# Kernel tuning notes

Hardware: AMD Instinct MI355X
Metric: run time of the kernel (lower is better)

Reference implementation:

```python
import jax, jax.numpy as jnp
import numpy as np

H = 4  # pairwise_num_attention_heads

def _layer_norm(x, gamma, beta, eps=1e-5):
    mu = jnp.mean(x, axis=-1, keepdims=True)
    var = jnp.var(x, axis=-1, keepdims=True)
    return (x - mu) * jax.lax.rsqrt(var + eps) * gamma + beta

def setup_inputs() -> dict:
    key = jax.random.key(0)
    ks = jax.random.split(key, 8)
    B, L, P = 1, 256, 128
    s = 0.02
    return {
        "pairwise_states": jax.random.normal(ks[0], (B, L, L, P), jnp.float32),
        "ln_gamma": jnp.ones((P,), jnp.float32),
        "ln_beta": jnp.zeros((P,), jnp.float32),
        "Wq": jax.random.normal(ks[1], (P, P), jnp.float32) * s,
        "Wk": jax.random.normal(ks[2], (P, P), jnp.float32) * s,
        "Wv": jax.random.normal(ks[3], (P, P), jnp.float32) * s,
        "Wb": jax.random.normal(ks[4], (P, H), jnp.float32) * s,
        "Wg": jax.random.normal(ks[5], (P, P), jnp.float32) * s,
        "bg": jnp.zeros((P,), jnp.float32),
        "Wo": jax.random.normal(ks[6], (P, P), jnp.float32) * s,
        "bo": jnp.zeros((P,), jnp.float32),
    }

def reference(pairwise_states, ln_gamma, ln_beta, Wq, Wk, Wv, Wb, Wg, bg, Wo, bo):
    # Row-axis triangle attention (RibonanzaNetPairwiseAttention, axis='row', eval mode).
    B, L, _, P = pairwise_states.shape
    D = P // H  # attention_head_size
    x = _layer_norm(pairwise_states, ln_gamma, ln_beta)  # [b,i,j,p]
    q = (x @ Wq).reshape(B, L, L, H, D)
    k = (x @ Wk).reshape(B, L, L, H, D)
    v = (x @ Wv).reshape(B, L, L, H, D)
    scale = jnp.asarray(D, x.dtype) ** 0.5
    # pairwise bias: [b,i,j,h] -> broadcast over the row axis of the scores
    bias = jnp.einsum('bijp,ph->bhij', x, Wb)  # [b,h,L,L]
    # scores[b,h,i,j,k]: within row i, query position j attends to key position k
    scores = jnp.einsum('bijhd,bikhd->bhijk', q, k) / scale + bias[:, :, None]
    probs = jax.nn.softmax(scores, axis=-1)
    ctx = jnp.einsum('bhijk,bikhd->bijhd', probs, v).reshape(B, L, L, P)
    gate = jax.nn.sigmoid(x @ Wg + bg)
    ctx = gate * ctx
    # output dense + residual (AxisDropout is identity in eval mode)
    return ctx @ Wo + bo + pairwise_states
```

## Files before the change

### kernel.cpp

```cpp
#include <hip/hip_runtime.h>

#define NPOS 65536

typedef __attribute__((ext_vector_type(8))) short bf16x8;
typedef __attribute__((ext_vector_type(4))) float f32x4;

#if __has_builtin(__builtin_amdgcn_exp2f)
#define EXP2F(x) __builtin_amdgcn_exp2f(x)
#else
#define EXP2F(x) __expf((x) * 0.6931471805599453f)
#endif
#if __has_builtin(__builtin_amdgcn_rcpf)
#define RCPF(x) __builtin_amdgcn_rcpf(x)
#else
#define RCPF(x) (1.0f / (x))
#endif

static __device__ __forceinline__ unsigned short f2bf(float f) {
  union { float f; unsigned int u; } v; v.f = f;
  unsigned int r = v.u + 0x7fffu + ((v.u >> 16) & 1u);
  return (unsigned short)(r >> 16);
}
static __device__ __forceinline__ float lo_bf(unsigned int u) {
  union { unsigned int u; float f; } v; v.u = u << 16; return v.f;
}
static __device__ __forceinline__ float hi_bf(unsigned int u) {
  union { unsigned int u; float f; } v; v.u = u & 0xffff0000u; return v.f;
}
static __device__ __forceinline__ unsigned int permpack(float hi, float lo) {
  union { float f; unsigned int u; } a, b;
  a.f = hi; b.f = lo;
#if __has_builtin(__builtin_amdgcn_perm)
  return __builtin_amdgcn_perm(a.u, b.u, 0x07060302u);
#else
  return (a.u & 0xffff0000u) | (b.u >> 16);
#endif
}

__global__ void k_pack(const float* __restrict__ Wq, const float* __restrict__ Wk,
                       const float* __restrict__ Wv, const float* __restrict__ Wg,
                       const float* __restrict__ Wo,
                       ushort* __restrict__ WT, ushort* __restrict__ WoT) {
  int idx = blockIdx.x * blockDim.x + threadIdx.x;
  if (idx < 512 * 128) {
    int n = idx >> 7, k = idx & 127;
    int nn = n & 127;
    float val;
    if (n < 128)      val = Wq[k * 128 + nn] * (0.17677669529663687f * 1.4426950408889634f);
    else if (n < 256) val = Wk[k * 128 + nn];
    else if (n < 384) val = Wv[k * 128 + nn];
    else              val = Wg[k * 128 + nn];
    WT[idx] = f2bf(val);
  } else if (idx < 512 * 128 + 128 * 128) {
    int j = idx - 512 * 128;
    int n = j >> 7, k = j & 127;
    WoT[j] = f2bf(Wo[k * 128 + n]);
  }
}

__global__ __launch_bounds__(128, 4) void k_ln(
    const float* __restrict__ in, const float* __restrict__ gamma,
    const float* __restrict__ beta, const float* __restrict__ Wb,
    ushort* __restrict__ xln, ushort* __restrict__ biasB) {
  int t = threadIdx.x, wv = t >> 6, lane = t & 63;
  int n = lane & 15, g = lane >> 4;
  int myrow = blockIdx.x * 32 + wv * 16 + n;
  const float* rp = in + (size_t)myrow * 128;

  float xv[32];
  float sm = 0.f, ssm = 0.f;
  #pragma unroll
  for (int kc = 0; kc < 4; kc++)
    #pragma unroll
    for (int pr = 0; pr < 2; pr++) {
      float4 v = *(const float4*)(rp + kc * 32 + g * 8 + pr * 4);
      int o = kc * 8 + pr * 4;
      xv[o] = v.x; xv[o+1] = v.y; xv[o+2] = v.z; xv[o+3] = v.w;
      sm  += v.x + v.y + v.z + v.w;
      ssm += v.x*v.x + v.y*v.y + v.z*v.z + v.w*v.w;
    }
  sm  += __shfl_xor(sm, 16, 64);  sm  += __shfl_xor(sm, 32, 64);
  ssm += __shfl_xor(ssm, 16, 64); ssm += __shfl_xor(ssm, 32, 64);
  float mu  = sm * (1.0f / 128.0f);
  float var = ssm * (1.0f / 128.0f) - mu * mu;
  float rs  = rsqrtf(var + 1e-5f);
  float p0 = 0.f, p1 = 0.f, p2 = 0.f, p3 = 0.f;
  #pragma unroll
  for (int kc = 0; kc < 4; kc++)
    #pragma unroll
    for (int pr = 0; pr < 2; pr++) {
      int c0 = kc * 32 + g * 8 + pr * 4;
      float4 g4 = *(const float4*)(gamma + c0);
      float4 b4 = *(const float4*)(beta + c0);
      int o = kc * 8 + pr * 4;
      #pragma unroll
      for (int r = 0; r < 4; r++) {
        float xn = (xv[o + r] - mu) * rs * (&g4.x)[r] + (&b4.x)[r];
        xv[o + r] = xn;
        float4 w = ((const float4*)Wb)[c0 + r];
        p0 += xn * w.x; p1 += xn * w.y; p2 += xn * w.z; p3 += xn * w.w;
      }
    }
  #pragma unroll
  for (int kc = 0; kc < 4; kc++)
    #pragma unroll
    for (int pr = 0; pr < 2; pr++) {
      int o = kc * 8 + pr * 4;
      uint2 px;
      px.x = (unsigned int)f2bf(xv[o]) | ((unsigned int)f2bf(xv[o + 1]) << 16);
      px.y = (unsigned int)f2bf(xv[o + 2]) | ((unsigned int)f2bf(xv[o + 3]) << 16);
      *(uint2*)(xln + (size_t)myrow * 128 + kc * 32 + g * 8 + pr * 4) = px;
    }
  p0 += __shfl_xor(p0, 16, 64); p0 += __shfl_xor(p0, 32, 64);
  p1 += __shfl_xor(p1, 16, 64); p1 += __shfl_xor(p1, 32, 64);
  p2 += __shfl_xor(p2, 16, 64); p2 += __shfl_xor(p2, 32, 64);
  p3 += __shfl_xor(p3, 16, 64); p3 += __shfl_xor(p3, 32, 64);
  if (g == 0) {
    const float l2e = 1.4426950408889634f;
    biasB[0 * NPOS + myrow] = f2bf(p0 * l2e);
    biasB[1 * NPOS + myrow] = f2bf(p1 * l2e);
    biasB[2 * NPOS + myrow] = f2bf(p2 * l2e);
    biasB[3 * NPOS + myrow] = f2bf(p3 * l2e);
  }
}

#define KS 36
#define VS 264
#define QS 36
__global__ __launch_bounds__(512, 3) void k_attn2(
    const ushort* __restrict__ xln, const ushort* __restrict__ WT,
    const float* __restrict__ bg, const ushort* __restrict__ biasB,
    ushort* __restrict__ gctx) {
  __shared__ __align__(16) ushort Klds[256 * KS];
  __shared__ __align__(16) ushort VTlds[32 * VS];
  __shared__ __align__(16) ushort qstg[8][32 * QS];
  int i = blockIdx.x & 255, h = blockIdx.x >> 8;
  int t = threadIdx.x, wv = t >> 6, lane = t & 63;
  int n = lane & 15, g = lane >> 4;
  int r0 = wv * 32;

  bf16x8 a[2][4];
  const ushort* xb = xln + ((size_t)i * 256 + r0) * 128;
  #pragma unroll
  for (int c = 0; c < 2; c++)
    #pragma unroll
    for (int kc = 0; kc < 4; kc++)
      a[c][kc] = *(const bf16x8*)(xb + (size_t)(c * 16 + n) * 128 + kc * 32 + g * 8);

  f32x4 gs[2][2];
  #pragma unroll
  for (int sect = 0; sect < 4; sect++) {
    bf16x8 b[2][4];
    #pragma unroll
    for (int ntl = 0; ntl < 2; ntl++)
      #pragma unroll
      for (int kc = 0; kc < 4; kc++)
        b[ntl][kc] = *(const bf16x8*)(WT + (size_t)(sect * 128 + h * 32 + ntl * 16 + n) * 128 + kc * 32 + g * 8);
    #pragma unroll
    for (int c = 0; c < 2; c++) {
      f32x4 acc[2];
      #pragma unroll
      for (int ntl = 0; ntl < 2; ntl++) {
        f32x4 cc = {0.f, 0.f, 0.f, 0.f};
        #pragma unroll
        for (int kc = 0; kc < 4; kc++)
          cc = __builtin_amdgcn_mfma_f32_16x16x32_bf16(a[c][kc], b[ntl][kc], cc, 0, 0, 0);
        acc[ntl] = cc;
      }
      if (sect == 0) {
        #pragma unroll
        for (int ntl = 0; ntl < 2; ntl++)
          #pragma unroll
          for (int r = 0; r < 4; r++)
            qstg[wv][(c * 16 + g * 4 + r) * QS + ntl * 16 + n] = f2bf(acc[ntl][r]);
      } else if (sect == 1) {
        #pragma unroll
        for (int ntl = 0; ntl < 2; ntl++)
          #pragma unroll
          for (int r = 0; r < 4; r++)
            Klds[(r0 + c * 16 + g * 4 + r) * KS + ntl * 16 + n] = f2bf(acc[ntl][r]);
      } else if (sect == 2) {
        #pragma unroll
        for (int ntl = 0; ntl < 2; ntl++) {
          uint2 vp;
          vp.x = (unsigned int)f2bf(acc[ntl][0]) | ((unsigned int)f2bf(acc[ntl][1]) << 16);
          vp.y = (unsigned int)f2bf(acc[ntl][2]) | ((unsigned int)f2bf(acc[ntl][3]) << 16);
          *(uint2*)(&VTlds[(ntl * 16 + n) * VS + r0 + c * 16 + g * 4]) = vp;
        }
      } else {
        #pragma unroll
        for (int ntl = 0; ntl < 2; ntl++)
          #pragma unroll
          for (int r = 0; r < 4; r++)
            gs[c][ntl][r] = 1.0f / (1.0f + __expf(-(acc[ntl][r] + bg[h * 32 + ntl * 16 + n])));
      }
    }
  }
  __syncthreads();

  const ushort* bb = biasB + (size_t)h * NPOS;
  #pragma unroll
  for (int tt = 0; tt < 2; tt++) {
    int j0 = r0 + tt * 16;
    union { bf16x8 v; uint2 u[2]; } bq;
    bq.u[0] = *(const uint2*)(&qstg[wv][(tt * 16 + n) * QS + g * 8]);
    bq.u[1] = *(const uint2*)(&qstg[wv][(tt * 16 + n) * QS + g * 8 + 4]);
    ushort* Pw = &qstg[wv][tt * 16 * QS];
    uint2 bv[16];
    #pragma unroll
    for (int kt = 0; kt < 16; kt++)
      bv[kt] = *(const uint2*)(bb + (size_t)(j0 + n) * 256 + kt * 16 + g * 4);
    f32x4 s[16];
    #pragma unroll
    for (int kt = 0; kt < 16; kt++) {
      union { bf16x8 v; uint2 u[2]; } ak;
      ak.u[0] = *(const uint2*)(&Klds[(kt * 16 + n) * KS + g * 8]);
      ak.u[1] = *(const uint2*)(&Klds[(kt * 16 + n) * KS + g * 8 + 4]);
      f32x4 cc;
      cc[0] = lo_bf(bv[kt].x); cc[1] = hi_bf(bv[kt].x);
      cc[2] = lo_bf(bv[kt].y); cc[3] = hi_bf(bv[kt].y);
      s[kt] = __builtin_amdgcn_mfma_f32_16x16x32_bf16(ak.v, bq.v, cc, 0, 0, 0);
    }
    f32x4 a4 = {0.f, 0.f, 0.f, 0.f};
    #pragma unroll
    for (int kt = 0; kt < 16; kt++) {
      #pragma unroll
      for (int r = 0; r < 4; r++) s[kt][r] = EXP2F(s[kt][r]);
      a4 += s[kt];
    }
    float smm = (a4[0] + a4[1]) + (a4[2] + a4[3]);
    smm += __shfl_xor(smm, 16, 64);
    smm += __shfl_xor(smm, 32, 64);
    float inv = RCPF(smm);
    f32x4 ctx0 = {0.f, 0.f, 0.f, 0.f}, ctx1 = {0.f, 0.f, 0.f, 0.f};
    #pragma unroll
    for (int c8 = 0; c8 < 8; c8++) {
      #pragma unroll
      for (int t2 = 0; t2 < 2; t2++) {
        int kt = c8 * 2 + t2;
        uint2 pp;
        pp.x = permpack(s[kt][1] * inv, s[kt][0] * inv);
        pp.y = permpack(s[kt][3] * inv, s[kt][2] * inv);
        *(uint2*)(&Pw[n * QS + t2 * 16 + g * 4]) = pp;
      }
      union { bf16x8 v; uint2 u[2]; } ap;
      ap.u[0] = *(const uint2*)(&Pw[n * QS + g * 8]);
      ap.u[1] = *(const uint2*)(&Pw[n * QS + g * 8 + 4]);
      bf16x8 v0 = *(const bf16x8*)(&VTlds[(size_t)n * VS + c8 * 32 + g * 8]);
      bf16x8 v1 = *(const bf16x8*)(&VTlds[(size_t)(16 + n) * VS + c8 * 32 + g * 8]);
      ctx0 = __builtin_amdgcn_mfma_f32_16x16x32_bf16(ap.v, v0, ctx0, 0, 0, 0);
      ctx1 = __builtin_amdgcn_mfma_f32_16x16x32_bf16(ap.v, v1, ctx1, 0, 0, 0);
    }
    #pragma unroll
    for (int r = 0; r < 4; r++) {
      size_t pos = (size_t)i * 256 + j0 + g * 4 + r;
      gctx[pos * 128 + h * 32 + n]      = f2bf(ctx0[r] * gs[tt][0][r]);
      gctx[pos * 128 + h * 32 + 16 + n] = f2bf(ctx1[r] * gs[tt][1][r]);
    }
  }
}

__global__ __launch_bounds__(256, 4) void k_out(
    const ushort* __restrict__ gctx, const ushort* __restrict__ WoT,
    const float* __restrict__ bo, const float* __restrict__ in0,
    float* __restrict__ out) {
  int t = threadIdx.x, wv = t >> 6, lane = t & 63;
  int n = lane & 15, g = lane >> 4;
  int row0 = blockIdx.x * 64 + wv * 16;
  bf16x8 cfr[4];
  #pragma unroll
  for (int kc = 0; kc < 4; kc++)
    cfr[kc] = *(const bf16x8*)(gctx + (size_t)(row0 + n) * 128 + kc * 32 + g * 8);
  size_t rowg = (size_t)row0 + n;
  #pragma unroll
  for (int ntl = 0; ntl < 8; ntl++) {
    f32x4 acc = {0.f, 0.f, 0.f, 0.f};
    #pragma unroll
    for (int kc = 0; kc < 4; kc++) {
      bf16x8 wo = *(const bf16x8*)(WoT + (size_t)(ntl * 16 + n) * 128 + kc * 32 + g * 8);
      acc = __builtin_amdgcn_mfma_f32_16x16x32_bf16(wo, cfr[kc], acc, 0, 0, 0);
    }
    f32x4 b4 = *(const f32x4*)(bo + ntl * 16 + g * 4);
    size_t o = rowg * 128 + ntl * 16 + g * 4;
    f32x4 r4 = *(const f32x4*)(in0 + o);
    acc[0] += b4[0] + r4[0]; acc[1] += b4[1] + r4[1];
    acc[2] += b4[2] + r4[2]; acc[3] += b4[3] + r4[3];
    *(f32x4*)(out + o) = acc;
  }
}

extern "C" void kernel_launch(void* const* d_in, const int* in_sizes, int n_in,
                              void* d_out, int out_size, void* d_ws, size_t ws_size,
                              hipStream_t stream) {
  const float* in0   = (const float*)d_in[0];
  const float* gamma = (const float*)d_in[1];
  const float* beta  = (const float*)d_in[2];
  const float* Wq    = (const float*)d_in[3];
  const float* Wk    = (const float*)d_in[4];
  const float* Wv    = (const float*)d_in[5];
  const float* Wb    = (const float*)d_in[6];
  const float* Wg    = (const float*)d_in[7];
  const float* bg    = (const float*)d_in[8];
  const float* Wo    = (const float*)d_in[9];
  const float* bo    = (const float*)d_in[10];
  float* out = (float*)d_out;
  char* ws = (char*)d_ws;

  const size_t MB = 1024 * 1024;
  ushort* gctx  = (ushort*)(ws);
  ushort* xln   = (ushort*)(ws + 16 * MB);
  ushort* biasB = (ushort*)(ws + 32 * MB);
  ushort* WT    = (ushort*)(ws + 33 * MB);
  ushort* WoT   = (ushort*)(ws + 33 * MB + 128 * 1024);

  k_pack <<<320, 256, 0, stream>>>(Wq, Wk, Wv, Wg, Wo, WT, WoT);
  k_ln   <<<2048, 128, 0, stream>>>(in0, gamma, beta, Wb, xln, biasB);
  k_attn2<<<1024, 512, 0, stream>>>(xln, WT, bg, biasB, gctx);
  k_out  <<<1024, 256, 0, stream>>>(gctx, WoT, bo, in0, out);
}
```

Baseline: 242.9 us.

## Keep Q in registers via transposed MFMA and shrink P staging

Computes the Q projection with swapped MFMA operands so its output lands directly in the register layout needed as the B operand for the scores MFMA. This removes the Q round trip through shared memory and its scalar stores. K is read with a permuted k-index layout (KS padded to 40) that stays consistent because the Q register packing matches. The P staging buffer shrinks to 16 rows with 16-byte loads. Occupancy hint drops from 3 to 2 blocks per SM, which may reduce latency hiding but allows more registers.

```diff
diff --git a/kernel.cpp b/kernel.cpp
--- a/kernel.cpp
+++ b/kernel.cpp
@@ -124,16 +124,16 @@
   }
 }
 
-#define KS 36
+#define KS 40
 #define VS 264
-#define QS 36
-__global__ __launch_bounds__(512, 3) void k_attn2(
+#define PST 40
+__global__ __launch_bounds__(512, 2) void k_attn2(
     const ushort* __restrict__ xln, const ushort* __restrict__ WT,
     const float* __restrict__ bg, const ushort* __restrict__ biasB,
     ushort* __restrict__ gctx) {
   __shared__ __align__(16) ushort Klds[256 * KS];
   __shared__ __align__(16) ushort VTlds[32 * VS];
-  __shared__ __align__(16) ushort qstg[8][32 * QS];
+  __shared__ __align__(16) ushort pstg[8][16 * PST];
   int i = blockIdx.x & 255, h = blockIdx.x >> 8;
   int t = threadIdx.x, wv = t >> 6, lane = t & 63;
   int n = lane & 15, g = lane >> 4;
@@ -147,6 +147,7 @@
     for (int kc = 0; kc < 4; kc++)
       a[c][kc] = *(const bf16x8*)(xb + (size_t)(c * 16 + n) * 128 + kc * 32 + g * 8);
 
+  bf16x8 qreg[2];
   f32x4 gs[2][2];
   #pragma unroll
   for (int sect = 0; sect < 4; sect++) {
@@ -163,16 +164,21 @@
       for (int ntl = 0; ntl < 2; ntl++) {
         f32x4 cc = {0.f, 0.f, 0.f, 0.f};
         #pragma unroll
-        for (int kc = 0; kc < 4; kc++)
-          cc = __builtin_amdgcn_mfma_f32_16x16x32_bf16(a[c][kc], b[ntl][kc], cc, 0, 0, 0);
+        for (int kc = 0; kc < 4; kc++) {
+          if (sect == 0)
+            cc = __builtin_amdgcn_mfma_f32_16x16x32_bf16(b[ntl][kc], a[c][kc], cc, 0, 0, 0);
+          else
+            cc = __builtin_amdgcn_mfma_f32_16x16x32_bf16(a[c][kc], b[ntl][kc], cc, 0, 0, 0);
+        }
         acc[ntl] = cc;
       }
       if (sect == 0) {
-        #pragma unroll
-        for (int ntl = 0; ntl < 2; ntl++)
-          #pragma unroll
-          for (int r = 0; r < 4; r++)
-            qstg[wv][(c * 16 + g * 4 + r) * QS + ntl * 16 + n] = f2bf(acc[ntl][r]);
+        union { bf16x8 v; uint2 u[2]; } q;
+        q.u[0].x = permpack(acc[0][1], acc[0][0]);
+        q.u[0].y = permpack(acc[0][3], acc[0][2]);
+        q.u[1].x = permpack(acc[1][1], acc[1][0]);
+        q.u[1].y = permpack(acc[1][3], acc[1][2]);
+        qreg[c] = q.v;
       } else if (sect == 1) {
         #pragma unroll
         for (int ntl = 0; ntl < 2; ntl++)
@@ -199,13 +205,10 @@
   __syncthreads();
 
   const ushort* bb = biasB + (size_t)h * NPOS;
+  ushort* Pw = pstg[wv];
   #pragma unroll
   for (int tt = 0; tt < 2; tt++) {
     int j0 = r0 + tt * 16;
-    union { bf16x8 v; uint2 u[2]; } bq;
-    bq.u[0] = *(const uint2*)(&qstg[wv][(tt * 16 + n) * QS + g * 8]);
-    bq.u[1] = *(const uint2*)(&qstg[wv][(tt * 16 + n) * QS + g * 8 + 4]);
-    ushort* Pw = &qstg[wv][tt * 16 * QS];
     uint2 bv[16];
     #pragma unroll
     for (int kt = 0; kt < 16; kt++)
@@ -214,12 +217,12 @@
     #pragma unroll
     for (int kt = 0; kt < 16; kt++) {
       union { bf16x8 v; uint2 u[2]; } ak;
-      ak.u[0] = *(const uint2*)(&Klds[(kt * 16 + n) * KS + g * 8]);
-      ak.u[1] = *(const uint2*)(&Klds[(kt * 16 + n) * KS + g * 8 + 4]);
+      ak.u[0] = *(const uint2*)(&Klds[(kt * 16 + n) * KS + g * 4]);
+      ak.u[1] = *(const uint2*)(&Klds[(kt * 16 + n) * KS + 16 + g * 4]);
       f32x4 cc;
       cc[0] = lo_bf(bv[kt].x); cc[1] = hi_bf(bv[kt].x);
       cc[2] = lo_bf(bv[kt].y); cc[3] = hi_bf(bv[kt].y);
-      s[kt] = __builtin_amdgcn_mfma_f32_16x16x32_bf16(ak.v, bq.v, cc, 0, 0, 0);
+      s[kt] = __builtin_amdgcn_mfma_f32_16x16x32_bf16(ak.v, qreg[tt], cc, 0, 0, 0);
     }
     f32x4 a4 = {0.f, 0.f, 0.f, 0.f};
     #pragma unroll
@@ -241,15 +244,13 @@
         uint2 pp;
         pp.x = permpack(s[kt][1] * inv, s[kt][0] * inv);
         pp.y = permpack(s[kt][3] * inv, s[kt][2] * inv);
-        *(uint2*)(&Pw[n * QS + t2 * 16 + g * 4]) = pp;
+        *(uint2*)(&Pw[n * PST + t2 * 16 + g * 4]) = pp;
       }
-      union { bf16x8 v; uint2 u[2]; } ap;
-      ap.u[0] = *(const uint2*)(&Pw[n * QS + g * 8]);
-      ap.u[1] = *(const uint2*)(&Pw[n * QS + g * 8 + 4]);
+      bf16x8 ap = *(const bf16x8*)(&Pw[n * PST + g * 8]);
       bf16x8 v0 = *(const bf16x8*)(&VTlds[(size_t)n * VS + c8 * 32 + g * 8]);
       bf16x8 v1 = *(const bf16x8*)(&VTlds[(size_t)(16 + n) * VS + c8 * 32 + g * 8]);
-      ctx0 = __builtin_amdgcn_mfma_f32_16x16x32_bf16(ap.v, v0, ctx0, 0, 0, 0);
-      ctx1 = __builtin_amdgcn_mfma_f32_16x16x32_bf16(ap.v, v1, ctx1, 0, 0, 0);
+      ctx0 = __builtin_amdgcn_mfma_f32_16x16x32_bf16(ap, v0, ctx0, 0, 0, 0);
+      ctx1 = __builtin_amdgcn_mfma_f32_16x16x32_bf16(ap, v1, ctx1, 0, 0, 0);
     }
     #pragma unroll
     for (int r = 0; r < 4; r++) {
```

Result: faster. 219.6 us (-9.6%).
